# Performance work log

Measured on AMD Instinct MI355X. Metric: run time of the kernel, lower is better.

## Reference

```python
import jax, jax.numpy as jnp
import numpy as np

B = 4096
D = 512
N_I = 1000000
N_T = 1000000
GAMMA = 0.8
EPS = 1e-10
RHO_I = 8.0
RHO_T = 8.0
ETA_INIT = 1e-05
BETA_U = 0.5
GRAD_CLIP = 5.0
TAU_MIN, TAU_MAX = 0.005, 0.05
TAU_INIT = 0.01


def setup_inputs() -> dict:
    key = jax.random.key(0)
    k1, k2 = jax.random.split(key)
    img = jax.random.normal(k1, (B, D), jnp.float32)
    txt = jax.random.normal(k2, (B, D), jnp.float32)
    # CLIP-style L2-normalized features
    img = img / jnp.linalg.norm(img, axis=1, keepdims=True)
    txt = txt / jnp.linalg.norm(txt, axis=1, keepdims=True)
    return {
        "image_features": img,
        "text_features": txt,
        "s_I": jnp.zeros(N_I, jnp.float32),
        "s_T": jnp.zeros(N_T, jnp.float32),
        "b_I": jnp.zeros(N_I, jnp.float32),
        "b_T": jnp.zeros(N_T, jnp.float32),
        "u_I": jnp.zeros(N_I, jnp.float32),
        "u_T": jnp.zeros(N_T, jnp.float32),
        "tau_I": jnp.full((N_I,), TAU_INIT, jnp.float32),
        "tau_T": jnp.full((N_T,), TAU_INIT, jnp.float32),
        "image_ids": jnp.arange(B, dtype=jnp.int32),
        "text_ids": jnp.arange(B, dtype=jnp.int32),
        "epoch": 1,
    }


def reference(image_features, text_features, s_I, s_T, b_I, b_T, u_I, u_T,
              tau_I, tau_T, image_ids, text_ids, epoch):
    sg = jax.lax.stop_gradient
    sim = jnp.einsum('id,jd->ij', image_features, text_features)  # [B,B]
    diag = jnp.diagonal(sim)
    Bn = sim.shape[0]
    tau_img = tau_I[image_ids]  # [B]
    tau_txt = tau_T[text_ids]   # [B]
    image_diffs = sim - diag[:, None]
    text_diffs = sim - diag[None, :]
    # .detach() in the original -> stop_gradient here
    idt = sg(image_diffs / tau_img[:, None])
    tdt = sg(text_diffs / tau_txt[None, :])
    old_b_I = b_I[image_ids]
    old_b_T = b_T[text_ids]
    # running max for log-sum-exp stabilization
    b_I_row = jnp.maximum(idt.max(axis=1), old_b_I)
    b_T_col = jnp.maximum(tdt.max(axis=0), old_b_T)
    b_I_new = b_I.at[image_ids].set(b_I_row)
    b_T_new = b_T.at[text_ids].set(b_T_col)
    mask = 1.0 - jnp.eye(Bn, dtype=sim.dtype)
    exp_i = jnp.exp(idt - b_I_row[:, None]) * mask
    exp_t = jnp.exp(tdt - b_T_col[None, :]) * mask
    g_I = exp_i.sum(axis=1)
    g_T = exp_t.sum(axis=0)
    if epoch == 0:
        sI = g_I
        sT = g_T
    else:
        sI = (1.0 - GAMMA) * s_I[image_ids] * jnp.exp(old_b_I - b_I_row) + GAMMA * g_I
        sT = (1.0 - GAMMA) * s_T[text_ids] * jnp.exp(old_b_T - b_T_col) + GAMMA * g_T
    s_I_new = s_I.at[image_ids].set(sI)
    s_T_new = s_T.at[text_ids].set(sT)
    w_i = sg(exp_i / (sI[:, None] + EPS))
    w_t = sg(exp_t / (sT[None, :] + EPS))
    image_loss = (w_i * image_diffs).sum(axis=1)
    text_loss = (w_t * text_diffs).sum(axis=0)
    total_loss = image_loss.mean() + text_loss.mean()
    tw_i = jnp.log(sI / (Bn - 1)) + b_I_row + RHO_I - (w_i * idt).sum(axis=1)
    tw_t = jnp.log(sT / (Bn - 1)) + b_T_col + RHO_T - (w_t * tdt).sum(axis=0)
    # torch uses in-place clamp_ on a view, so the returned means are clipped
    tw_i = jnp.clip(tw_i, -GRAD_CLIP, GRAD_CLIP)
    tw_t = jnp.clip(tw_t, -GRAD_CLIP, GRAD_CLIP)
    u_I_val = (1.0 - BETA_U) * u_I[image_ids] + BETA_U * tw_i
    u_T_val = (1.0 - BETA_U) * u_T[text_ids] + BETA_U * tw_t
    u_I_new = u_I.at[image_ids].set(u_I_val)
    u_T_new = u_T.at[text_ids].set(u_T_val)
    tau_I_new = tau_I.at[image_ids].set(jnp.clip(tau_img - ETA_INIT * u_I_val, TAU_MIN, TAU_MAX))
    tau_T_new = tau_T.at[text_ids].set(jnp.clip(tau_txt - ETA_INIT * u_T_val, TAU_MIN, TAU_MAX))
    return (total_loss, tau_img.mean(), tau_txt.mean(), tw_i.mean(), tw_t.mean(),
            s_I_new, s_T_new, b_I_new, b_T_new, u_I_new, u_T_new, tau_I_new, tau_T_new)
```

## Files before the change

### kernel.cpp

```cpp
#include <hip/hip_runtime.h>

typedef unsigned short u16;
typedef unsigned int u32;

typedef __bf16 bf16x8 __attribute__((ext_vector_type(8)));
typedef float floatx4 __attribute__((ext_vector_type(4)));

__device__ __forceinline__ u16 f2bf(float f) {
    union { float f; u32 u; } c; c.f = f;
    u32 u = c.u;
    u32 r = u + 0x7FFFu + ((u >> 16) & 1u);
    return (u16)(r >> 16);
}
__device__ __forceinline__ float bf2f(u16 x) {
    union { u32 u; float f; } c; c.u = ((u32)x) << 16; return c.f;
}

__device__ __forceinline__ void comb(float& M, float& P0, float& P1,
                                     float m, float p0, float p1) {
    float nm = fmaxf(M, m);
    float s = __expf(M - nm), t = __expf(m - nm);
    P0 = P0 * s + p0 * t;
    P1 = P1 * s + p1 * t;
    M = nm;
}

__device__ __forceinline__ void dma16(const u16* g, u16* l) {
#if __has_builtin(__builtin_amdgcn_global_load_lds)
    __builtin_amdgcn_global_load_lds(
        (const __attribute__((address_space(1))) u32*)g,
        (__attribute__((address_space(3))) u32*)l, 16, 0, 0);
#else
    int lane = threadIdx.x & 63;
    *(uint4*)(l + lane * 8) = *(const uint4*)(g);
#endif
}

__global__ __launch_bounds__(256) void presplit(
    const float* __restrict__ a, const float* __restrict__ b,
    u16* __restrict__ Ah, u16* __restrict__ Al,
    u16* __restrict__ Bh, u16* __restrict__ Bl, int n,
    const float* __restrict__ tauI, const float* __restrict__ tauT,
    const int* __restrict__ img_ids, const int* __restrict__ txt_ids,
    float* __restrict__ taur, float* __restrict__ tauc) {
    if (blockIdx.y == 0 && blockIdx.x < 16) {
        int t = blockIdx.x * 256 + threadIdx.x;
        taur[t] = tauI[img_ids[t]];
        tauc[t] = tauT[txt_ids[t]];
    }
    const float* src = blockIdx.y ? b : a;
    u16* dh = blockIdx.y ? Bh : Ah;
    u16* dl = blockIdx.y ? Bl : Al;
    int i = (blockIdx.x * 256 + threadIdx.x) * 8;
    if (i >= n) return;
    float4 v0 = *(const float4*)&src[i];
    float4 v1 = *(const float4*)&src[i + 4];
    float xs[8] = {v0.x, v0.y, v0.z, v0.w, v1.x, v1.y, v1.z, v1.w};
    u16 h[8], l[8];
#pragma unroll
    for (int e = 0; e < 8; e++) {
        h[e] = f2bf(xs[e]);
        l[e] = f2bf(xs[e] - bf2f(h[e]));
    }
    *(uint4*)&dh[i] = *(uint4*)h;
    *(uint4*)&dl[i] = *(uint4*)l;
}

#define COPY_BLOCKS 2048

__global__ __launch_bounds__(256) void gemm_flash(
    const u16* __restrict__ Ah, const u16* __restrict__ Al,
    const u16* __restrict__ Bh, const u16* __restrict__ Bl,
    const float* __restrict__ taur, const float* __restrict__ tauc,
    float* __restrict__ rowpart, float* __restrict__ colpart,
    float* __restrict__ diag,
    const float* __restrict__ p0, const float* __restrict__ p1,
    const float* __restrict__ p2, const float* __restrict__ p3,
    const float* __restrict__ p4, const float* __restrict__ p5,
    const float* __restrict__ p6, const float* __restrict__ p7,
    float* __restrict__ out, long long n) {
    __shared__ __align__(16) u16 smem[4 * 128 * 32];
    u16* sAh = smem;
    u16* sAl = smem + 4096;
    u16* sBh = smem + 8192;
    u16* sBl = smem + 12288;
    float* redbuf = (float*)smem;

    const int bid = blockIdx.x;
    if (bid >= 1024) {
        const int cb = bid - 1024;
        const int k = cb >> 8, blk = cb & 255;
        const float* srcs[8] = {p0, p1, p2, p3, p4, p5, p6, p7};
        const float* src = srcs[k];
        float* dst = out + 5 + (size_t)k * (size_t)n;
        const long long G = (n - 3) >> 2;
        for (long long g = (long long)blk * 256 + threadIdx.x; g < G;
             g += 256 * 256) {
            long long e = 3 + 4 * g;
            float4 q = {src[e], src[e + 1], src[e + 2], src[e + 3]};
            *(float4*)&dst[e] = q;
        }
        if (blk == 0) {
            int t = threadIdx.x;
            long long tail0 = 3 + 4 * G;
            int tcount = (int)(n - tail0);
            if (t < 3) dst[t] = src[t];
            else if (t < 3 + tcount) dst[tail0 + (t - 3)] = src[tail0 + (t - 3)];
        }
        return;
    }

    const int tid  = threadIdx.x;
    const int wave = tid >> 6, lane = tid & 63;
    const int lr = lane & 15, quad = lane >> 4;
    const int waveM = wave >> 1, waveN = wave & 1;
    const int rowtile = bid >> 5, coltile = bid & 31;
    const int rowBase = rowtile * 128;
    const int colBase = coltile * 128;

    const int o0 = wave * 1024 + lane * 16;
    const int o1 = o0 + 4096;
    const int r0s = o0 >> 6, c0s = (o0 & 63) >> 1;
    const int r1s = o1 >> 6, c1s = (o1 & 63) >> 1;
    const int l0 = wave * 512;
    const int l1 = wave * 512 + 2048;

    floatx4 acc[4][4];
#pragma unroll
    for (int mi = 0; mi < 4; mi++)
#pragma unroll
        for (int ni = 0; ni < 4; ni++) acc[mi][ni] = (floatx4)0.0f;

    for (int k0 = 0; k0 < 512; k0 += 32) {
        __syncthreads();
        dma16(&Ah[(size_t)(rowBase + r0s) * 512 + k0 + c0s], sAh + l0);
        dma16(&Ah[(size_t)(rowBase + r1s) * 512 + k0 + c1s], sAh + l1);
        dma16(&Al[(size_t)(rowBase + r0s) * 512 + k0 + c0s], sAl + l0);
        dma16(&Al[(size_t)(rowBase + r1s) * 512 + k0 + c1s], sAl + l1);
        dma16(&Bh[(size_t)(colBase + r0s) * 512 + k0 + c0s], sBh + l0);
        dma16(&Bh[(size_t)(colBase + r1s) * 512 + k0 + c1s], sBh + l1);
        dma16(&Bl[(size_t)(colBase + r0s) * 512 + k0 + c0s], sBl + l0);
        dma16(&Bl[(size_t)(colBase + r1s) * 512 + k0 + c1s], sBl + l1);
        __syncthreads();

        bf16x8 afh[4], afl[4], bfh[4], bfl[4];
#pragma unroll
        for (int mi = 0; mi < 4; mi++) {
            int off = (waveM * 64 + mi * 16 + lr) * 32 + quad * 8;
            afh[mi] = *(const bf16x8*)&sAh[off];
            afl[mi] = *(const bf16x8*)&sAl[off];
        }
#pragma unroll
        for (int ni = 0; ni < 4; ni++) {
            int off = (waveN * 64 + ni * 16 + lr) * 32 + quad * 8;
            bfh[ni] = *(const bf16x8*)&sBh[off];
            bfl[ni] = *(const bf16x8*)&sBl[off];
        }
#pragma unroll
        for (int mi = 0; mi < 4; mi++)
#pragma unroll
            for (int ni = 0; ni < 4; ni++) {
                acc[mi][ni] = __builtin_amdgcn_mfma_f32_16x16x32_bf16(afh[mi], bfh[ni], acc[mi][ni], 0, 0, 0);
                acc[mi][ni] = __builtin_amdgcn_mfma_f32_16x16x32_bf16(afh[mi], bfl[ni], acc[mi][ni], 0, 0, 0);
                acc[mi][ni] = __builtin_amdgcn_mfma_f32_16x16x32_bf16(afl[mi], bfh[ni], acc[mi][ni], 0, 0, 0);
            }
    }
    __syncthreads();


    if (rowtile == coltile && waveM == waveN) {
#pragma unroll
        for (int mi = 0; mi < 4; mi++)
#pragma unroll
            for (int r = 0; r < 4; r++)
                if (lr == quad * 4 + r)
                    diag[colBase + waveN * 64 + mi * 16 + lr] = acc[mi][mi][r];
    }

#pragma unroll
    for (int mi = 0; mi < 4; mi++) {
#pragma unroll
        for (int r = 0; r < 4; r++) {
            int row_local = waveM * 64 + mi * 16 + quad * 4 + r;
            float vmax = fmaxf(fmaxf(acc[mi][0][r], acc[mi][1][r]),
                               fmaxf(acc[mi][2][r], acc[mi][3][r]));
#pragma unroll
            for (int mask = 1; mask <= 8; mask <<= 1)
                vmax = fmaxf(vmax, __shfl_xor(vmax, mask));
            float it = 1.0f / taur[rowBase + row_local];
            float M = vmax * it;
            float P0 = 0.f, P1 = 0.f;
#pragma unroll
            for (int ni = 0; ni < 4; ni++) {
                float y = acc[mi][ni][r] * it;
                float e = __expf(y - M);
                P0 += e;
                P1 += y * e;
            }
#pragma unroll
            for (int mask = 1; mask <= 8; mask <<= 1) {
                P0 += __shfl_xor(P0, mask);
                P1 += __shfl_xor(P1, mask);
            }
            if (lr == 0) {
                int x = (row_local * 2 + waveN) * 3;
                redbuf[x] = M; redbuf[x + 1] = P0; redbuf[x + 2] = P1;
            }
        }
    }

#pragma unroll
    for (int ni = 0; ni < 4; ni++) {
        int col_local = waveN * 64 + ni * 16 + lr;
        float vmax = -3.4e38f;
#pragma unroll
        for (int mi = 0; mi < 4; mi++)
            vmax = fmaxf(vmax,
                fmaxf(fmaxf(acc[mi][ni][0], acc[mi][ni][1]),
                      fmaxf(acc[mi][ni][2], acc[mi][ni][3])));
#pragma unroll
        for (int mask = 16; mask <= 32; mask <<= 1)
            vmax = fmaxf(vmax, __shfl_xor(vmax, mask));
        float it = 1.0f / tauc[colBase + col_local];
        float M = vmax * it;
        float P0 = 0.f, P1 = 0.f;
#pragma unroll
        for (int mi = 0; mi < 4; mi++)
#pragma unroll
            for (int r = 0; r < 4; r++) {
                float y = acc[mi][ni][r] * it;
                float e = __expf(y - M);
                P0 += e;
                P1 += y * e;
            }
#pragma unroll
        for (int mask = 16; mask <= 32; mask <<= 1) {
            P0 += __shfl_xor(P0, mask);
            P1 += __shfl_xor(P1, mask);
        }
        if (quad == 0) {
            int x = 768 + (col_local * 2 + waveM) * 3;
            redbuf[x] = M; redbuf[x + 1] = P0; redbuf[x + 2] = P1;
        }
    }
    __syncthreads();

    if (tid < 128) {
        int x = tid * 6;
        float M = redbuf[x], P0 = redbuf[x + 1], P1 = redbuf[x + 2];
        comb(M, P0, P1, redbuf[x + 3], redbuf[x + 4], redbuf[x + 5]);
        float* dst = &rowpart[(size_t)(rowBase + tid) * 96 + coltile * 3];
        dst[0] = M; dst[1] = P0; dst[2] = P1;
    } else {
        int c = tid - 128;
        int x = 768 + c * 6;
        float M = redbuf[x], P0 = redbuf[x + 1], P1 = redbuf[x + 2];
        comb(M, P0, P1, redbuf[x + 3], redbuf[x + 4], redbuf[x + 5]);
        float* dst = &colpart[(size_t)(colBase + c) * 96 + rowtile * 3];
        dst[0] = M; dst[1] = P0; dst[2] = P1;
    }
}

struct FinArgs {
    const float* rowpart; const float* colpart; const float* diag;
    const float* tauI; const float* sI; const float* bI; const float* uI;
    const float* tauT; const float* sT; const float* bT; const float* uT;
    const int* img_ids; const int* txt_ids; const int* epoch_p;
    float* out; float* rowbuf; long long n;
};

__global__ __launch_bounds__(256) void rows_final(FinArgs a) {
    int t = blockIdx.x * 256 + threadIdx.x;
    int side = t >> 12, i = t & 4095;
    const float* part   = side ? a.colpart : a.rowpart;
    const int*   ids    = side ? a.txt_ids : a.img_ids;
    const float* tau_in = side ? a.tauT : a.tauI;
    const float* s_in   = side ? a.sT   : a.sI;
    const float* b_in   = side ? a.bT   : a.bI;
    const float* u_in   = side ? a.uT   : a.uI;

    const float* p = part + (size_t)i * 96;
    float M = -3.4e38f, P0 = 0.f, P1 = 0.f;
#pragma unroll 4
    for (int k = 0; k < 32; k++)
        comb(M, P0, P1, p[3 * k], p[3 * k + 1], p[3 * k + 2]);

    const int id = ids[i];
    const float tau   = tau_in[id];
    const float old_b = b_in[id];
    const float old_s = s_in[id];
    const float old_u = u_in[id];
    const float y_ii  = a.diag[i] / tau;

    float b_row = fmaxf(M - y_ii, old_b);
    float e  = expf(M - y_ii - b_row);
    float S0 = P0 * e - expf(-b_row);
    float S1 = (P1 - y_ii * P0) * e;

    float g = S0;
    float sI = (*a.epoch_p == 0) ? g
             : 0.2f * old_s * expf(old_b - b_row) + 0.8f * g;
    float denom = sI + 1e-10f;
    float wsum = S1 / denom;
    float lossr = tau * wsum;
    float tw = logf(sI * (1.0f / 4095.0f)) + b_row + 8.0f - wsum;
    tw = fminf(fmaxf(tw, -5.0f), 5.0f);
    float uval = 0.5f * old_u + 0.5f * tw;
    float taun = fminf(fmaxf(tau - 1e-5f * uval, 0.005f), 0.05f);

    float* sect = a.out + 5;
    sect[(size_t)(0 + side) * (size_t)a.n + id] = sI;
    sect[(size_t)(2 + side) * (size_t)a.n + id] = b_row;
    sect[(size_t)(4 + side) * (size_t)a.n + id] = uval;
    sect[(size_t)(6 + side) * (size_t)a.n + id] = taun;

    a.rowbuf[(2 * side + 0) * 4096 + i] = lossr;
    a.rowbuf[(2 * side + 1) * 4096 + i] = tw;
}

__global__ __launch_bounds__(256) void scalars(
    const float* __restrict__ rows,
    const float* __restrict__ tau_I, const float* __restrict__ tau_T,
    const int* __restrict__ image_ids, const int* __restrict__ text_ids,
    float* __restrict__ out) {
    int tid = threadIdx.x;
    int lane = tid & 63, wv = tid >> 6;
    float a[6] = {0, 0, 0, 0, 0, 0};
    for (int e = tid; e < 4096; e += 256) {
        a[0] += rows[0 * 4096 + e];
        a[1] += rows[1 * 4096 + e];
        a[2] += rows[2 * 4096 + e];
        a[3] += rows[3 * 4096 + e];
        a[4] += tau_I[image_ids[e]];
        a[5] += tau_T[text_ids[e]];
    }
    __shared__ float sred[4][6];
#pragma unroll
    for (int k = 0; k < 6; k++)
        for (int o = 32; o > 0; o >>= 1) a[k] += __shfl_xor(a[k], o);
    if (lane == 0)
#pragma unroll
        for (int k = 0; k < 6; k++) sred[wv][k] = a[k];
    __syncthreads();
    if (tid == 0) {
#pragma unroll
        for (int k = 0; k < 6; k++)
            a[k] = sred[0][k] + sred[1][k] + sred[2][k] + sred[3][k];
        const float inv = 1.0f / 4096.0f;
        out[0] = (a[0] + a[2]) * inv;
        out[1] = a[4] * inv;
        out[2] = a[5] * inv;
        out[3] = a[1] * inv;
        out[4] = a[3] * inv;
    }
}

extern "C" void kernel_launch(void* const* d_in, const int* in_sizes, int n_in,
                              void* d_out, int out_size, void* d_ws, size_t ws_size,
                              hipStream_t stream) {
    const float* img   = (const float*)d_in[0];
    const float* txt   = (const float*)d_in[1];
    const float* s_I   = (const float*)d_in[2];
    const float* s_T   = (const float*)d_in[3];
    const float* b_I   = (const float*)d_in[4];
    const float* b_T   = (const float*)d_in[5];
    const float* u_I   = (const float*)d_in[6];
    const float* u_T   = (const float*)d_in[7];
    const float* tau_I = (const float*)d_in[8];
    const float* tau_T = (const float*)d_in[9];
    const int* image_ids = (const int*)d_in[10];
    const int* text_ids  = (const int*)d_in[11];
    const int* epoch     = (const int*)d_in[12];
    float* out = (float*)d_out;
    const long long n = in_sizes[2];
    const int nfeat = in_sizes[0];

    const size_t MB = 1024 * 1024;
    u16* Ah = (u16*)d_ws;
    u16* Al = Ah + (size_t)nfeat;
    u16* Bh = Al + (size_t)nfeat;
    u16* Bl = Bh + (size_t)nfeat;
    float* rowpart = (float*)((char*)d_ws + 16 * MB);
    float* colpart = (float*)((char*)d_ws + 18 * MB);
    float* diag    = (float*)((char*)d_ws + 20 * MB);
    float* taur    = (float*)((char*)d_ws + 20 * MB + 256 * 1024);
    float* tauc    = (float*)((char*)d_ws + 20 * MB + 512 * 1024);
    float* rows    = (float*)((char*)d_ws + 21 * MB);

    presplit<<<dim3((nfeat / 8 + 255) / 256, 2), 256, 0, stream>>>(
        img, txt, Ah, Al, Bh, Bl, nfeat,
        tau_I, tau_T, image_ids, text_ids, taur, tauc);

    gemm_flash<<<1024 + COPY_BLOCKS, 256, 0, stream>>>(
        Ah, Al, Bh, Bl, taur, tauc, rowpart, colpart, diag,
        s_I, s_T, b_I, b_T, u_I, u_T, tau_I, tau_T, out, n);

    FinArgs fa;
    fa.rowpart = rowpart; fa.colpart = colpart; fa.diag = diag;
    fa.tauI = tau_I; fa.sI = s_I; fa.bI = b_I; fa.uI = u_I;
    fa.tauT = tau_T; fa.sT = s_T; fa.bT = b_T; fa.uT = u_T;
    fa.img_ids = image_ids; fa.txt_ids = text_ids; fa.epoch_p = epoch;
    fa.out = out; fa.rowbuf = rows; fa.n = n;
    rows_final<<<32, 256, 0, stream>>>(fa);

    scalars<<<1, 256, 0, stream>>>(rows, tau_I, tau_T, image_ids, text_ids, out);
}
```

Before: 203.3 us.

## Pre-swizzle bf16 splits into MFMA fragment layout and load directly from global

The presplit kernel now writes hi/lo bf16 arrays in a fragment-tiled layout, so each 16-row by 32-k MFMA fragment is contiguous per lane. The GEMM drops the LDS staging and its barriers and loads operand fragments straight from global memory with coalesced 16-byte loads. This removes the LDS round trip and synchronisation, but loses reuse across waves: each wave now fetches its own A and B fragments from global/L2, which raises memory traffic and exposes load latency with little prefetching.

```diff
diff --git a/kernel.cpp b/kernel.cpp
--- a/kernel.cpp
+++ b/kernel.cpp
@@ -23,17 +23,6 @@
     P0 = P0 * s + p0 * t;
     P1 = P1 * s + p1 * t;
     M = nm;
-}
-
-__device__ __forceinline__ void dma16(const u16* g, u16* l) {
-#if __has_builtin(__builtin_amdgcn_global_load_lds)
-    __builtin_amdgcn_global_load_lds(
-        (const __attribute__((address_space(1))) u32*)g,
-        (__attribute__((address_space(3))) u32*)l, 16, 0, 0);
-#else
-    int lane = threadIdx.x & 63;
-    *(uint4*)(l + lane * 8) = *(const uint4*)(g);
-#endif
 }
 
 __global__ __launch_bounds__(256) void presplit(
@@ -62,8 +51,10 @@
         h[e] = f2bf(xs[e]);
         l[e] = f2bf(xs[e] - bf2f(h[e]));
     }
-    *(uint4*)&dh[i] = *(uint4*)h;
-    *(uint4*)&dl[i] = *(uint4*)l;
+    int r = i >> 9, k = i & 511;
+    int off = (((r >> 4) << 4) + (k >> 5)) * 512 + ((((k >> 3) & 3) << 4) + (r & 15)) * 8;
+    *(uint4*)&dh[off] = *(uint4*)h;
+    *(uint4*)&dl[off] = *(uint4*)l;
 }
 
 #define COPY_BLOCKS 2048
@@ -79,12 +70,7 @@
     const float* __restrict__ p4, const float* __restrict__ p5,
     const float* __restrict__ p6, const float* __restrict__ p7,
     float* __restrict__ out, long long n) {
-    __shared__ __align__(16) u16 smem[4 * 128 * 32];
-    u16* sAh = smem;
-    u16* sAl = smem + 4096;
-    u16* sBh = smem + 8192;
-    u16* sBl = smem + 12288;
-    float* redbuf = (float*)smem;
+    __shared__ float redbuf[1536];
 
     const int bid = blockIdx.x;
     if (bid >= 1024) {
@@ -118,12 +104,8 @@
     const int rowBase = rowtile * 128;
     const int colBase = coltile * 128;
 
-    const int o0 = wave * 1024 + lane * 16;
-    const int o1 = o0 + 4096;
-    const int r0s = o0 >> 6, c0s = (o0 & 63) >> 1;
-    const int r1s = o1 >> 6, c1s = (o1 & 63) >> 1;
-    const int l0 = wave * 512;
-    const int l1 = wave * 512 + 2048;
+    const size_t baseA = ((size_t)((rowBase >> 4) + waveM * 4)) * 8192 + lane * 8;
+    const size_t baseB = ((size_t)((colBase >> 4) + waveN * 4)) * 8192 + lane * 8;
 
     floatx4 acc[4][4];
 #pragma unroll
@@ -131,30 +113,20 @@
 #pragma unroll
         for (int ni = 0; ni < 4; ni++) acc[mi][ni] = (floatx4)0.0f;
 
-    for (int k0 = 0; k0 < 512; k0 += 32) {
-        __syncthreads();
-        dma16(&Ah[(size_t)(rowBase + r0s) * 512 + k0 + c0s], sAh + l0);
-        dma16(&Ah[(size_t)(rowBase + r1s) * 512 + k0 + c1s], sAh + l1);
-        dma16(&Al[(size_t)(rowBase + r0s) * 512 + k0 + c0s], sAl + l0);
-        dma16(&Al[(size_t)(rowBase + r1s) * 512 + k0 + c1s], sAl + l1);
-        dma16(&Bh[(size_t)(colBase + r0s) * 512 + k0 + c0s], sBh + l0);
-        dma16(&Bh[(size_t)(colBase + r1s) * 512 + k0 + c1s], sBh + l1);
-        dma16(&Bl[(size_t)(colBase + r0s) * 512 + k0 + c0s], sBl + l0);
-        dma16(&Bl[(size_t)(colBase + r1s) * 512 + k0 + c1s], sBl + l1);
-        __syncthreads();
-
+#pragma unroll 2
+    for (int tk = 0; tk < 16; tk++) {
         bf16x8 afh[4], afl[4], bfh[4], bfl[4];
 #pragma unroll
         for (int mi = 0; mi < 4; mi++) {
-            int off = (waveM * 64 + mi * 16 + lr) * 32 + quad * 8;
-            afh[mi] = *(const bf16x8*)&sAh[off];
-            afl[mi] = *(const bf16x8*)&sAl[off];
+            size_t off = baseA + (size_t)mi * 8192 + tk * 512;
+            afh[mi] = *(const bf16x8*)&Ah[off];
+            afl[mi] = *(const bf16x8*)&Al[off];
         }
 #pragma unroll
         for (int ni = 0; ni < 4; ni++) {
-            int off = (waveN * 64 + ni * 16 + lr) * 32 + quad * 8;
-            bfh[ni] = *(const bf16x8*)&sBh[off];
-            bfl[ni] = *(const bf16x8*)&sBl[off];
+            size_t off = baseB + (size_t)ni * 8192 + tk * 512;
+            bfh[ni] = *(const bf16x8*)&Bh[off];
+            bfl[ni] = *(const bf16x8*)&Bl[off];
         }
 #pragma unroll
         for (int mi = 0; mi < 4; mi++)
@@ -165,7 +137,6 @@
                 acc[mi][ni] = __builtin_amdgcn_mfma_f32_16x16x32_bf16(afl[mi], bfh[ni], acc[mi][ni], 0, 0, 0);
             }
     }
-    __syncthreads();
 
 
     if (rowtile == coltile && waveM == waveN) {
```

After: 205.9 us. Within noise of the previous version (+1.3%).
